# Kernel optimization log

Measured on AMD Instinct MI355X. Metric: run time of the kernel, lower is better.

Reference implementation:

```python
import jax, jax.numpy as jnp
import numpy as np

N = 100000
MUL = 16


def _build_cg():
    # Real-basis Clebsch-Gordan (Wigner-3j-style) coefficients, shape (2l1+1, 2l2+1, 2lo+1),
    # each normalized to unit Frobenius norm per output component (e3nn component normalization).
    eps = np.zeros((3, 3, 3), np.float32)
    for a, b, c in [(0, 1, 2), (1, 2, 0), (2, 0, 1)]:
        eps[a, b, c] = 1.0
        eps[a, c, b] = -1.0
    s2 = np.float32(1.0 / np.sqrt(2.0))
    q = np.zeros((5, 3, 3), np.float32)  # l=2 real harmonics: xy, yz, 3z^2-r^2, xz, x^2-y^2
    q[0, 0, 1] = q[0, 1, 0] = s2
    q[1, 1, 2] = q[1, 2, 1] = s2
    q[2] = np.diag([-1.0, -1.0, 2.0]).astype(np.float32) / np.sqrt(6.0)
    q[3, 0, 2] = q[3, 2, 0] = s2
    q[4] = np.diag([1.0, -1.0, 0.0]).astype(np.float32) * s2
    cg000 = jnp.ones((1, 1, 1), jnp.float32)                                   # 0e x 0e -> 0e
    cg011 = jnp.asarray(np.eye(3, dtype=np.float32)[None])                      # 0e x 1o -> 1o
    cg110 = jnp.asarray((np.eye(3, dtype=np.float32) / np.sqrt(3.0))[:, :, None])  # 1o x 1o -> 0e
    cg111 = jnp.asarray(eps * s2)                                               # 1o x 1o -> 1e
    cg112 = jnp.asarray(np.transpose(q, (1, 2, 0)))                             # 1o x 1o -> 2e
    return cg000, cg011, cg110, cg111, cg112


def _path(x1, x2, cg, w, alpha):
    # 'uvw' tensor-product path: out[z,w,m] = alpha * sum_{u,v,i,j} x1[z,u,i] x2[z,v,j] cg[i,j,m] w[u,v,w]
    # Contraction order chosen to keep the largest intermediate at [z,u,w,j].
    t = jnp.einsum('zvj,uvw->zuwj', x2, w)
    s = jnp.einsum('zui,zuwj->zwij', x1, t)
    return alpha * jnp.einsum('zwij,ijm->zwm', s, cg)


def _tensor_square(x, w0, w1, w2, w3, w4):
    n = x.shape[0]
    x0 = x[:, :MUL].reshape(n, MUL, 1)       # 16x0e
    x1 = x[:, MUL:].reshape(n, MUL, 3)       # 16x1o
    cg000, cg011, cg110, cg111, cg112 = _build_cg()
    a2 = 1.0 / np.sqrt(MUL * MUL * 2.0)      # 0e output receives 2 paths
    a1 = 1.0 / np.sqrt(MUL * MUL * 1.0)
    o_0e = _path(x0, x0, cg000, w0, a2) + _path(x1, x1, cg110, w2, a2)
    o_1o = _path(x0, x1, cg011, w1, a1)
    o_1e = _path(x1, x1, cg111, w3, a1)
    o_2e = _path(x1, x1, cg112, w4, a1)
    return jnp.concatenate([o.reshape(n, -1) for o in (o_0e, o_1o, o_1e, o_2e)], axis=1)


def setup_inputs() -> dict:
    key = jax.random.key(0)
    kx, k0, k1, k2, k3, k4 = jax.random.split(key, 6)
    return {
        'x': jax.random.normal(kx, (N, MUL * 1 + MUL * 3), jnp.float32),
        'w0': jax.random.normal(k0, (MUL, MUL, MUL), jnp.float32),
        'w1': jax.random.normal(k1, (MUL, MUL, MUL), jnp.float32),
        'w2': jax.random.normal(k2, (MUL, MUL, MUL), jnp.float32),
        'w3': jax.random.normal(k3, (MUL, MUL, MUL), jnp.float32),
        'w4': jax.random.normal(k4, (MUL, MUL, MUL), jnp.float32),
    }


def reference(x, w0, w1, w2, w3, w4):
    return _tensor_square(x, w0, w1, w2, w3, w4)
```

## Files before the change

kernel.cpp:

```cpp
#include <hip/hip_runtime.h>
#include <hip/hip_bf16.h>

typedef __attribute__((ext_vector_type(8))) short short8;
typedef __attribute__((ext_vector_type(4))) float float4v;
typedef __attribute__((ext_vector_type(2))) float float2v;
typedef __attribute__((ext_vector_type(4))) unsigned uint4v;

#define S_A 0.04419417382415922f
#define S_B 0.025515518153991442f
#define S_C 0.0625f

static __device__ __forceinline__ unsigned pkbf(float a, float b) {
    unsigned r;
    asm("v_cvt_pk_bf16_f32 %0, %1, %2" : "=v"(r) : "v"(a), "v"(b));
    return r;
}

__global__ void wprep_kernel(const float* __restrict__ wA, const float* __restrict__ wB,
                             const float* __restrict__ wC, const float* __restrict__ wD,
                             const float* __restrict__ wE, unsigned short* __restrict__ wout)
{
    int e = blockIdx.x * 256 + threadIdx.x;
    if (e >= 5 * 4096) return;
    int p = e >> 12;
    int rem = e & 4095;
    const float* wp = (p == 0) ? wA : (p == 1) ? wB : (p == 2) ? wC : (p == 3) ? wD : wE;
    unsigned u = __builtin_bit_cast(unsigned, wp[rem]);
    u += 0x7fffu + ((u >> 16) & 1u);
    int k = rem >> 4, w = rem & 15;
    int c = k >> 5, kk = k & 31;
    int lane = ((kk >> 3) << 4) | w;
    int j = kk & 7;
    wout[(((c * 5 + p) * 64 + lane) << 3) | j] = (unsigned short)(u >> 16);
}

template<int G>
static __device__ __forceinline__ int pathof(int i) {
    if constexpr (G == 0) return (i == 0) ? 0 : (i == 1) ? 1 : 4;
    if constexpr (G == 1) return (i == 0) ? 2 : (i == 1) ? 3 : 4;
    return (i == 0) ? 3 : 4;
}

template<int G>
static __device__ __forceinline__ void run_group(
    const float* __restrict__ xr, int l, const short8* __restrict__ wbase,
    float* __restrict__ out, long long z0)
{
    const int r  = l & 15;
    const int g  = l >> 4;
    const int v0 = (g & 1) * 8;
    const int uo = g >> 1;

    float2v Xv[4], Yv[4], Zv[4];
    float2v A0v[4];
    {
        float b[24];
        #pragma unroll
        for (int q = 0; q < 6; q++)
            *(float4v*)&b[q * 4] = *(const float4v*)(xr + 16 + v0 * 3 + q * 4);
        #pragma unroll
        for (int t = 0; t < 4; t++) {
            Xv[t] = (float2v){b[6 * t + 0], b[6 * t + 3]};
            Yv[t] = (float2v){b[6 * t + 1], b[6 * t + 4]};
            Zv[t] = (float2v){b[6 * t + 2], b[6 * t + 5]};
        }
        if constexpr (G == 0) {
            float a[8];
            #pragma unroll
            for (int q = 0; q < 2; q++)
                *(float4v*)&a[q * 4] = *(const float4v*)(xr + v0 + q * 4);
            #pragma unroll
            for (int t = 0; t < 4; t++) A0v[t] = (float2v){a[2 * t], a[2 * t + 1]};
        }
    }

    constexpr int NS = (G == 1) ? 5 : 4;
    constexpr int NP = (G == 2) ? 2 : 3;

    float4v acc[NS];
    #pragma unroll
    for (int s = 0; s < NS; s++) acc[s] = (float4v){0.f, 0.f, 0.f, 0.f};

    #pragma unroll
    for (int c = 0; c < 8; c++) {
        short8 wf[NP];
        #pragma unroll
        for (int i = 0; i < NP; i++) wf[i] = wbase[(c * 5 + pathof<G>(i)) * 64 + l];

        const int u = c * 2 + uo;
        float u0 = 0.f, ux = 0.f, uy, uz;
        if constexpr (G != 2) u0 = xr[u];
        if constexpr (G != 1) ux = xr[16 + u * 3 + 0];
        uy = xr[16 + u * 3 + 1];
        uz = xr[16 + u * 3 + 2];

        unsigned fri[NS][4];
        #pragma unroll
        for (int t = 0; t < 4; t++) {
            const float2v X = Xv[t], Y = Yv[t], Z = Zv[t];
            if constexpr (G == 0) {
                float2v b0  = u0 * A0v[t];
                float2v p00 = ux * X, p11 = uy * Y, p22 = uz * Z;
                float2v t01 = p00 + p11;
                float2v b1  = t01 + p22;
                float2v b10 = 2.0f * p22 - t01;
                float2v b12 = p00 - p11;
                fri[0][t] = pkbf(b0.x, b0.y);
                fri[1][t] = pkbf(b1.x, b1.y);
                fri[2][t] = pkbf(b10.x, b10.y);
                fri[3][t] = pkbf(b12.x, b12.y);
            }
            if constexpr (G == 1) {
                float2v b2 = u0 * X, b3 = u0 * Y, b4 = u0 * Z;
                float2v p12 = uy * Z;
                float2v b5 = p12 - uz * Y;
                float2v b9 = p12 + uz * Y;
                fri[0][t] = pkbf(b2.x, b2.y);
                fri[1][t] = pkbf(b3.x, b3.y);
                fri[2][t] = pkbf(b4.x, b4.y);
                fri[3][t] = pkbf(b5.x, b5.y);
                fri[4][t] = pkbf(b9.x, b9.y);
            }
            if constexpr (G == 2) {
                float2v p01 = ux * Y;
                float2v b7  = p01 - uy * X;
                float2v b8  = p01 + uy * X;
                float2v p02 = ux * Z;
                float2v b6  = uz * X - p02;
                float2v b11 = p02 + uz * X;
                fri[0][t] = pkbf(b6.x, b6.y);
                fri[1][t] = pkbf(b7.x, b7.y);
                fri[2][t] = pkbf(b8.x, b8.y);
                fri[3][t] = pkbf(b11.x, b11.y);
            }
        }

        #pragma unroll
        for (int s = 0; s < NS; s++) {
            short8 frm = __builtin_bit_cast(short8, *(uint4v*)fri[s]);
            int wi;
            if constexpr (G == 0) wi = (s == 0) ? 0 : (s == 1) ? 1 : 2;
            if constexpr (G == 1) wi = (s <= 2) ? 0 : (s == 3) ? 1 : 2;
            if constexpr (G == 2) wi = (s <= 1) ? 0 : 1;
            acc[s] = __builtin_amdgcn_mfma_f32_16x16x32_bf16(frm, wf[wi], acc[s], 0, 0, 0);
        }
    }

    const int w = r;
    float* outp = out + (z0 + g * 4) * 192;
    #pragma unroll
    for (int reg = 0; reg < 4; reg++) {
        float* rowp = outp + reg * 192;
        if constexpr (G == 0) {
            rowp[w]               = S_A * acc[0][reg] + S_B * acc[1][reg];
            rowp[112 + w * 5 + 2] = S_B * acc[2][reg];
            rowp[112 + w * 5 + 4] = S_A * acc[3][reg];
        }
        if constexpr (G == 1) {
            rowp[16 + w * 3 + 0]  = S_C * acc[0][reg];
            rowp[16 + w * 3 + 1]  = S_C * acc[1][reg];
            rowp[16 + w * 3 + 2]  = S_C * acc[2][reg];
            rowp[64 + w * 3 + 0]  = S_A * acc[3][reg];
            rowp[112 + w * 5 + 1] = S_A * acc[4][reg];
        }
        if constexpr (G == 2) {
            rowp[64 + w * 3 + 1]  = S_A * acc[0][reg];
            rowp[64 + w * 3 + 2]  = S_A * acc[1][reg];
            rowp[112 + w * 5 + 0] = S_A * acc[2][reg];
            rowp[112 + w * 5 + 3] = S_A * acc[3][reg];
        }
    }
}

__global__ __launch_bounds__(192, 4)
void tsq_kernel(const float* __restrict__ x,
                const unsigned short* __restrict__ wfrag,
                float* __restrict__ out,
                int nrows)
{
    __shared__ __attribute__((aligned(16))) float xlds[16 * 68];

    const int tid = threadIdx.x;
    const long long z0 = (long long)blockIdx.x * 16;

    {
        const float* xg = x + z0 * 64;
        {
            int f = tid * 4;
            int row = f >> 6, col = f & 63;
            float4v v = {0.f, 0.f, 0.f, 0.f};
            if (z0 + row < nrows) v = *(const float4v*)(xg + f);
            *(float4v*)&xlds[row * 68 + col] = v;
        }
        if (tid < 64) {
            int f = 768 + tid * 4;
            int row = f >> 6, col = f & 63;
            float4v v = {0.f, 0.f, 0.f, 0.f};
            if (z0 + row < nrows) v = *(const float4v*)(xg + f);
            *(float4v*)&xlds[row * 68 + col] = v;
        }
    }
    __syncthreads();
    if (z0 >= nrows) return;

    const int wave = tid >> 6;
    const int l = tid & 63;
    const float* xr = &xlds[(l & 15) * 68];
    const short8* wbase = (const short8*)wfrag;

    if      (wave == 0) run_group<0>(xr, l, wbase, out, z0);
    else if (wave == 1) run_group<1>(xr, l, wbase, out, z0);
    else                run_group<2>(xr, l, wbase, out, z0);
}

extern "C" void kernel_launch(void* const* d_in, const int* in_sizes, int n_in,
                              void* d_out, int out_size, void* d_ws, size_t ws_size,
                              hipStream_t stream) {
    const float* x  = (const float*)d_in[0];
    const float* w0 = (const float*)d_in[1];
    const float* w1 = (const float*)d_in[2];
    const float* w2 = (const float*)d_in[3];
    const float* w3 = (const float*)d_in[4];
    const float* w4 = (const float*)d_in[5];
    float* out = (float*)d_out;
    unsigned short* wfrag = (unsigned short*)d_ws;
    (void)ws_size; (void)n_in; (void)out_size;

    const int nrows = in_sizes[0] / 64;
    const int nblocks = (nrows + 15) / 16;

    wprep_kernel<<<dim3(80), dim3(256), 0, stream>>>(w0, w2, w1, w3, w4, wfrag);
    tsq_kernel<<<dim3(nblocks), dim3(192), 0, stream>>>(x, wfrag, out, nrows);
}
```

Before: 123.7 us.

## Process two 16-row tiles per block, reusing weight fragments across both

Each block now handles 32 rows instead of 16. Every wave loads its bf16 weight fragments once per chunk and feeds them to MFMAs for both row halves, which halves weight-fragment global loads per row and the number of blocks. It also interleaves two independent accumulation chains for more instruction-level parallelism, and adds row bounds checks on the stores. The cost is higher register use (launch bounds lowered to 3 blocks per CU) and fewer blocks overall.

```diff
diff --git a/kernel.cpp b/kernel.cpp
--- a/kernel.cpp
+++ b/kernel.cpp
@@ -43,26 +43,29 @@
 
 template<int G>
 static __device__ __forceinline__ void run_group(
-    const float* __restrict__ xr, int l, const short8* __restrict__ wbase,
-    float* __restrict__ out, long long z0)
+    const float* __restrict__ xrA, const float* __restrict__ xrB,
+    int l, const short8* __restrict__ wbase,
+    float* __restrict__ out, long long z0, int nrows)
 {
-    const int r  = l & 15;
+    const int w  = l & 15;
     const int g  = l >> 4;
     const int v0 = (g & 1) * 8;
     const int uo = g >> 1;
 
-    float2v Xv[4], Yv[4], Zv[4];
-    float2v A0v[4];
-    {
+    float2v Xv[2][4], Yv[2][4], Zv[2][4];
+    float2v A0v[2][4];
+    #pragma unroll
+    for (int h = 0; h < 2; h++) {
+        const float* xr = h ? xrB : xrA;
         float b[24];
         #pragma unroll
         for (int q = 0; q < 6; q++)
             *(float4v*)&b[q * 4] = *(const float4v*)(xr + 16 + v0 * 3 + q * 4);
         #pragma unroll
         for (int t = 0; t < 4; t++) {
-            Xv[t] = (float2v){b[6 * t + 0], b[6 * t + 3]};
-            Yv[t] = (float2v){b[6 * t + 1], b[6 * t + 4]};
-            Zv[t] = (float2v){b[6 * t + 2], b[6 * t + 5]};
+            Xv[h][t] = (float2v){b[6 * t + 0], b[6 * t + 3]};
+            Yv[h][t] = (float2v){b[6 * t + 1], b[6 * t + 4]};
+            Zv[h][t] = (float2v){b[6 * t + 2], b[6 * t + 5]};
         }
         if constexpr (G == 0) {
             float a[8];
@@ -70,16 +73,18 @@
             for (int q = 0; q < 2; q++)
                 *(float4v*)&a[q * 4] = *(const float4v*)(xr + v0 + q * 4);
             #pragma unroll
-            for (int t = 0; t < 4; t++) A0v[t] = (float2v){a[2 * t], a[2 * t + 1]};
+            for (int t = 0; t < 4; t++) A0v[h][t] = (float2v){a[2 * t], a[2 * t + 1]};
         }
     }
 
     constexpr int NS = (G == 1) ? 5 : 4;
     constexpr int NP = (G == 2) ? 2 : 3;
 
-    float4v acc[NS];
-    #pragma unroll
-    for (int s = 0; s < NS; s++) acc[s] = (float4v){0.f, 0.f, 0.f, 0.f};
+    float4v acc[2][NS];
+    #pragma unroll
+    for (int h = 0; h < 2; h++)
+        #pragma unroll
+        for (int s = 0; s < NS; s++) acc[h][s] = (float4v){0.f, 0.f, 0.f, 0.f};
 
     #pragma unroll
     for (int c = 0; c < 8; c++) {
@@ -87,101 +92,108 @@
         #pragma unroll
         for (int i = 0; i < NP; i++) wf[i] = wbase[(c * 5 + pathof<G>(i)) * 64 + l];
 
-        const int u = c * 2 + uo;
-        float u0 = 0.f, ux = 0.f, uy, uz;
-        if constexpr (G != 2) u0 = xr[u];
-        if constexpr (G != 1) ux = xr[16 + u * 3 + 0];
-        uy = xr[16 + u * 3 + 1];
-        uz = xr[16 + u * 3 + 2];
-
-        unsigned fri[NS][4];
-        #pragma unroll
-        for (int t = 0; t < 4; t++) {
-            const float2v X = Xv[t], Y = Yv[t], Z = Zv[t];
+        #pragma unroll
+        for (int h = 0; h < 2; h++) {
+            const float* xr = h ? xrB : xrA;
+            const int u = c * 2 + uo;
+            float u0 = 0.f, ux = 0.f, uy, uz;
+            if constexpr (G != 2) u0 = xr[u];
+            if constexpr (G != 1) ux = xr[16 + u * 3 + 0];
+            uy = xr[16 + u * 3 + 1];
+            uz = xr[16 + u * 3 + 2];
+
+            unsigned fri[NS][4];
+            #pragma unroll
+            for (int t = 0; t < 4; t++) {
+                const float2v X = Xv[h][t], Y = Yv[h][t], Z = Zv[h][t];
+                if constexpr (G == 0) {
+                    float2v b0  = u0 * A0v[h][t];
+                    float2v p00 = ux * X, p11 = uy * Y, p22 = uz * Z;
+                    float2v t01 = p00 + p11;
+                    float2v b1  = t01 + p22;
+                    float2v b10 = 2.0f * p22 - t01;
+                    float2v b12 = p00 - p11;
+                    fri[0][t] = pkbf(b0.x, b0.y);
+                    fri[1][t] = pkbf(b1.x, b1.y);
+                    fri[2][t] = pkbf(b10.x, b10.y);
+                    fri[3][t] = pkbf(b12.x, b12.y);
+                }
+                if constexpr (G == 1) {
+                    float2v b2 = u0 * X, b3 = u0 * Y, b4 = u0 * Z;
+                    float2v p12 = uy * Z;
+                    float2v b5 = p12 - uz * Y;
+                    float2v b9 = p12 + uz * Y;
+                    fri[0][t] = pkbf(b2.x, b2.y);
+                    fri[1][t] = pkbf(b3.x, b3.y);
+                    fri[2][t] = pkbf(b4.x, b4.y);
+                    fri[3][t] = pkbf(b5.x, b5.y);
+                    fri[4][t] = pkbf(b9.x, b9.y);
+                }
+                if constexpr (G == 2) {
+                    float2v p01 = ux * Y;
+                    float2v b7  = p01 - uy * X;
+                    float2v b8  = p01 + uy * X;
+                    float2v p02 = ux * Z;
+                    float2v b6  = uz * X - p02;
+                    float2v b11 = p02 + uz * X;
+                    fri[0][t] = pkbf(b6.x, b6.y);
+                    fri[1][t] = pkbf(b7.x, b7.y);
+                    fri[2][t] = pkbf(b8.x, b8.y);
+                    fri[3][t] = pkbf(b11.x, b11.y);
+                }
+            }
+
+            #pragma unroll
+            for (int s = 0; s < NS; s++) {
+                short8 frm = __builtin_bit_cast(short8, *(uint4v*)fri[s]);
+                int wi;
+                if constexpr (G == 0) wi = (s == 0) ? 0 : (s == 1) ? 1 : 2;
+                if constexpr (G == 1) wi = (s <= 2) ? 0 : (s == 3) ? 1 : 2;
+                if constexpr (G == 2) wi = (s <= 1) ? 0 : 1;
+                acc[h][s] = __builtin_amdgcn_mfma_f32_16x16x32_bf16(frm, wf[wi], acc[h][s], 0, 0, 0);
+            }
+        }
+    }
+
+    #pragma unroll
+    for (int h = 0; h < 2; h++) {
+        #pragma unroll
+        for (int reg = 0; reg < 4; reg++) {
+            long long rowz = z0 + h * 16 + g * 4 + reg;
+            if (rowz >= nrows) continue;
+            float* rowp = out + rowz * 192;
             if constexpr (G == 0) {
-                float2v b0  = u0 * A0v[t];
-                float2v p00 = ux * X, p11 = uy * Y, p22 = uz * Z;
-                float2v t01 = p00 + p11;
-                float2v b1  = t01 + p22;
-                float2v b10 = 2.0f * p22 - t01;
-                float2v b12 = p00 - p11;
-                fri[0][t] = pkbf(b0.x, b0.y);
-                fri[1][t] = pkbf(b1.x, b1.y);
-                fri[2][t] = pkbf(b10.x, b10.y);
-                fri[3][t] = pkbf(b12.x, b12.y);
+                rowp[w]               = S_A * acc[h][0][reg] + S_B * acc[h][1][reg];
+                rowp[112 + w * 5 + 2] = S_B * acc[h][2][reg];
+                rowp[112 + w * 5 + 4] = S_A * acc[h][3][reg];
             }
             if constexpr (G == 1) {
-                float2v b2 = u0 * X, b3 = u0 * Y, b4 = u0 * Z;
-                float2v p12 = uy * Z;
-                float2v b5 = p12 - uz * Y;
-                float2v b9 = p12 + uz * Y;
-                fri[0][t] = pkbf(b2.x, b2.y);
-                fri[1][t] = pkbf(b3.x, b3.y);
-                fri[2][t] = pkbf(b4.x, b4.y);
-                fri[3][t] = pkbf(b5.x, b5.y);
-                fri[4][t] = pkbf(b9.x, b9.y);
+                rowp[16 + w * 3 + 0]  = S_C * acc[h][0][reg];
+                rowp[16 + w * 3 + 1]  = S_C * acc[h][1][reg];
+                rowp[16 + w * 3 + 2]  = S_C * acc[h][2][reg];
+                rowp[64 + w * 3 + 0]  = S_A * acc[h][3][reg];
+                rowp[112 + w * 5 + 1] = S_A * acc[h][4][reg];
             }
             if constexpr (G == 2) {
-                float2v p01 = ux * Y;
-                float2v b7  = p01 - uy * X;
-                float2v b8  = p01 + uy * X;
-                float2v p02 = ux * Z;
-                float2v b6  = uz * X - p02;
-                float2v b11 = p02 + uz * X;
-                fri[0][t] = pkbf(b6.x, b6.y);
-                fri[1][t] = pkbf(b7.x, b7.y);
-                fri[2][t] = pkbf(b8.x, b8.y);
-                fri[3][t] = pkbf(b11.x, b11.y);
-            }
-        }
-
-        #pragma unroll
-        for (int s = 0; s < NS; s++) {
-            short8 frm = __builtin_bit_cast(short8, *(uint4v*)fri[s]);
-            int wi;
-            if constexpr (G == 0) wi = (s == 0) ? 0 : (s == 1) ? 1 : 2;
-            if constexpr (G == 1) wi = (s <= 2) ? 0 : (s == 3) ? 1 : 2;
-            if constexpr (G == 2) wi = (s <= 1) ? 0 : 1;
-            acc[s] = __builtin_amdgcn_mfma_f32_16x16x32_bf16(frm, wf[wi], acc[s], 0, 0, 0);
-        }
-    }
-
-    const int w = r;
-    float* outp = out + (z0 + g * 4) * 192;
-    #pragma unroll
-    for (int reg = 0; reg < 4; reg++) {
-        float* rowp = outp + reg * 192;
-        if constexpr (G == 0) {
-            rowp[w]               = S_A * acc[0][reg] + S_B * acc[1][reg];
-            rowp[112 + w * 5 + 2] = S_B * acc[2][reg];
-            rowp[112 + w * 5 + 4] = S_A * acc[3][reg];
-        }
-        if constexpr (G == 1) {
-            rowp[16 + w * 3 + 0]  = S_C * acc[0][reg];
-            rowp[16 + w * 3 + 1]  = S_C * acc[1][reg];
-            rowp[16 + w * 3 + 2]  = S_C * acc[2][reg];
-            rowp[64 + w * 3 + 0]  = S_A * acc[3][reg];
-            rowp[112 + w * 5 + 1] = S_A * acc[4][reg];
-        }
-        if constexpr (G == 2) {
-            rowp[64 + w * 3 + 1]  = S_A * acc[0][reg];
-            rowp[64 + w * 3 + 2]  = S_A * acc[1][reg];
-            rowp[112 + w * 5 + 0] = S_A * acc[2][reg];
-            rowp[112 + w * 5 + 3] = S_A * acc[3][reg];
-        }
-    }
-}
-
-__global__ __launch_bounds__(192, 4)
+                rowp[64 + w * 3 + 1]  = S_A * acc[h][0][reg];
+                rowp[64 + w * 3 + 2]  = S_A * acc[h][1][reg];
+                rowp[112 + w * 5 + 0] = S_A * acc[h][2][reg];
+                rowp[112 + w * 5 + 3] = S_A * acc[h][3][reg];
+            }
+        }
+    }
+}
+
+__global__ __launch_bounds__(192, 3)
 void tsq_kernel(const float* __restrict__ x,
                 const unsigned short* __restrict__ wfrag,
                 float* __restrict__ out,
                 int nrows)
 {
-    __shared__ __attribute__((aligned(16))) float xlds[16 * 68];
+    __shared__ __attribute__((aligned(16))) float xlds[32 * 68];
 
     const int tid = threadIdx.x;
-    const long long z0 = (long long)blockIdx.x * 16;
+    const long long z0 = (long long)blockIdx.x * 32;
 
     {
         const float* xg = x + z0 * 64;
@@ -192,25 +204,33 @@
             if (z0 + row < nrows) v = *(const float4v*)(xg + f);
             *(float4v*)&xlds[row * 68 + col] = v;
         }
-        if (tid < 64) {
+        {
             int f = 768 + tid * 4;
             int row = f >> 6, col = f & 63;
             float4v v = {0.f, 0.f, 0.f, 0.f};
             if (z0 + row < nrows) v = *(const float4v*)(xg + f);
             *(float4v*)&xlds[row * 68 + col] = v;
         }
+        if (tid < 128) {
+            int f = 1536 + tid * 4;
+            int row = f >> 6, col = f & 63;
+            float4v v = {0.f, 0.f, 0.f, 0.f};
+            if (z0 + row < nrows) v = *(const float4v*)(xg + f);
+            *(float4v*)&xlds[row * 68 + col] = v;
+        }
     }
     __syncthreads();
     if (z0 >= nrows) return;
 
     const int wave = tid >> 6;
     const int l = tid & 63;
-    const float* xr = &xlds[(l & 15) * 68];
+    const float* xrA = &xlds[(l & 15) * 68];
+    const float* xrB = &xlds[((l & 15) + 16) * 68];
     const short8* wbase = (const short8*)wfrag;
 
-    if      (wave == 0) run_group<0>(xr, l, wbase, out, z0);
-    else if (wave == 1) run_group<1>(xr, l, wbase, out, z0);
-    else                run_group<2>(xr, l, wbase, out, z0);
+    if      (wave == 0) run_group<0>(xrA, xrB, l, wbase, out, z0, nrows);
+    else if (wave == 1) run_group<1>(xrA, xrB, l, wbase, out, z0, nrows);
+    else                run_group<2>(xrA, xrB, l, wbase, out, z0, nrows);
 }
 
 extern "C" void kernel_launch(void* const* d_in, const int* in_sizes, int n_in,
@@ -227,7 +247,7 @@
     (void)ws_size; (void)n_in; (void)out_size;
 
     const int nrows = in_sizes[0] / 64;
-    const int nblocks = (nrows + 15) / 16;
+    const int nblocks = (nrows + 31) / 32;
 
     wprep_kernel<<<dim3(80), dim3(256), 0, stream>>>(w0, w2, w1, w3, w4, wfrag);
     tsq_kernel<<<dim3(nblocks), dim3(192), 0, stream>>>(x, wfrag, out, nrows);
```

After: 123.8 us. Within noise of the previous version (+0.0%).
